# Kernel optimization log

Measured on AMD Instinct MI355X. Metric: run time of the kernel, lower is better.

Reference implementation:

```python
import jax, jax.numpy as jnp
import numpy as np

N, D, H, E, K = 8192, 1024, 4096, 8, 2


def setup_inputs() -> dict:
    key = jax.random.key(0)
    ks = jax.random.split(key, 4)
    scaled = lambda k, shp, fan: (jax.random.normal(k, shp, jnp.float32) / np.sqrt(fan).astype(np.float32))
    return {
        "x": jax.random.normal(ks[0], (N, D), jnp.float32),
        "Wg": scaled(ks[1], (D, E), D),
        "bg": jnp.zeros((E,), jnp.float32),
        "W1": scaled(ks[2], (E, D, H), D),
        "b1": jnp.zeros((E, H), jnp.float32),
        "W2": scaled(ks[3], (E, H, D), H),
        "b2": jnp.zeros((E, D), jnp.float32),
    }


def reference(x, Wg, bg, W1, b1, W2, b2):
    # Gating: softmax over experts, top-k selection, renormalize top-k probs.
    gate_probs = jax.nn.softmax(x @ Wg + bg, axis=-1)            # [N, E]
    topk_p, topk_i = jax.lax.top_k(gate_probs, K)                # [N, K]
    topk_p = topk_p / topk_p.sum(axis=-1, keepdims=True)
    onehot = jax.nn.one_hot(topk_i, E, dtype=x.dtype)            # [N, K, E]
    # Per-token combine weight for each expert (0 if expert not in top-k).
    w = (onehot * topk_p[..., None]).sum(axis=1)                 # [N, E]

    out = jnp.zeros_like(x)
    for e in range(E):  # fixed small loop over structurally distinct experts
        h = jax.nn.relu(x @ W1[e] + b1[e])                       # dropout = identity (eval)
        out = out + w[:, e:e + 1] * (h @ W2[e] + b2[e])

    # Load-balancing auxiliary loss.
    importance = gate_probs.sum(axis=0)
    importance = importance / importance.sum()
    load = onehot.sum(axis=(0, 1)) / (x.shape[0] * K)            # [E]
    lb_loss = E * (importance * load).sum()
    return out, lb_loss
```

## Files before the change

kernel.cpp:

```cpp
#include <hip/hip_runtime.h>
#include <hip/hip_bf16.h>
#include <math.h>

#define NTOK 8192
#define DDIM 1024
#define HDIM 4096
#define NEXP 8
#define KTOP 2
#define MAXROWS 17408
#define MAXTILES 136

typedef __bf16 bf16x8 __attribute__((ext_vector_type(8)));
typedef float f32x4 __attribute__((ext_vector_type(4)));

#define GAS __attribute__((address_space(1)))
#define LAS __attribute__((address_space(3)))

__device__ __forceinline__ void async16(const void* g, void* l) {
  __builtin_amdgcn_global_load_lds((GAS void*)g, (LAS void*)l, 16, 0, 0);
}

#define XB_OFF     ((size_t)0)
#define W1T_OFF    (XB_OFF + (size_t)NTOK*DDIM*2)
#define ROWOUT_OFF W1T_OFF
#define W2T_OFF    (W1T_OFF + (size_t)NEXP*DDIM*HDIM*2)
#define HB_OFF     (W2T_OFF + (size_t)NEXP*HDIM*DDIM*2)
#define ROWTOK_OFF (HB_OFF + (size_t)MAXROWS*HDIM*2)
#define ROWW_OFF   (ROWTOK_OFF + (size_t)MAXROWS*4)
#define TOKE_OFF   (ROWW_OFF + (size_t)MAXROWS*4)
#define TOKW_OFF   (TOKE_OFF + (size_t)NTOK*KTOP*4)
#define TOKROW_OFF (TOKW_OFF + (size_t)NTOK*KTOP*4)
#define TILEE_OFF  (TOKROW_OFF + (size_t)NTOK*KTOP*4)
#define CNT_OFF    (TILEE_OFF + (size_t)256*4)
#define POS_OFF    (CNT_OFF + 64)
#define IMP_OFF    (POS_OFF + 64)
#define META_OFF   (IMP_OFF + 64)

__global__ void init_kernel(int* counts, float* importance) {
  if (threadIdx.x < NEXP) { counts[threadIdx.x] = 0; importance[threadIdx.x] = 0.f; }
}

__global__ void cast_x_kernel(const float* __restrict__ src, __hip_bfloat16* __restrict__ dst) {
  size_t i = ((size_t)blockIdx.x * blockDim.x + threadIdx.x) * 4;
  if (i < (size_t)NTOK * DDIM) {
    float4 v = *(const float4*)(src + i);
    dst[i + 0] = __float2bfloat16(v.x);
    dst[i + 1] = __float2bfloat16(v.y);
    dst[i + 2] = __float2bfloat16(v.z);
    dst[i + 3] = __float2bfloat16(v.w);
  }
}

__global__ __launch_bounds__(256) void transpose_cast_kernel(
    const float* __restrict__ src, __hip_bfloat16* __restrict__ dst, int R, int C) {
  __shared__ float tile[64][65];
  const int e = blockIdx.z;
  const float* s = src + (size_t)e * R * C;
  __hip_bfloat16* d = dst + (size_t)e * R * C;
  const int c0 = blockIdx.x * 64, r0 = blockIdx.y * 64;
  const int tc = (threadIdx.x & 15) * 4;
  const int tr = threadIdx.x >> 4;
#pragma unroll
  for (int p = 0; p < 4; ++p) {
    float4 v = *(const float4*)&s[(size_t)(r0 + tr + p * 16) * C + c0 + tc];
    tile[tr + p * 16][tc + 0] = v.x;
    tile[tr + p * 16][tc + 1] = v.y;
    tile[tr + p * 16][tc + 2] = v.z;
    tile[tr + p * 16][tc + 3] = v.w;
  }
  __syncthreads();
  const int oc = threadIdx.x >> 4;
  const int orr = (threadIdx.x & 15) * 4;
#pragma unroll
  for (int p = 0; p < 4; ++p) {
    const int c = oc + p * 16;
    __hip_bfloat16 tmp[4];
    tmp[0] = __float2bfloat16(tile[orr + 0][c]);
    tmp[1] = __float2bfloat16(tile[orr + 1][c]);
    tmp[2] = __float2bfloat16(tile[orr + 2][c]);
    tmp[3] = __float2bfloat16(tile[orr + 3][c]);
    *(ushort4*)&d[(size_t)(c0 + c) * R + r0 + orr] = *(ushort4*)tmp;
  }
}

__global__ __launch_bounds__(256) void gating_kernel(
    const float* __restrict__ x, const float* __restrict__ Wg, const float* __restrict__ bg,
    int* __restrict__ tok_e, float* __restrict__ tok_w,
    int* __restrict__ counts, float* __restrict__ importance) {
  const int tid = threadIdx.x, wid = tid >> 6, lane = tid & 63;
  const int t = blockIdx.x * 32 + wid * 8 + (lane >> 3);
  const int e = lane & 7;
  const float* xr = x + (size_t)t * DDIM;
  double dot = 0.0;
  for (int d = 0; d < DDIM; d += 4) {
    float4 xv = *(const float4*)(xr + d);
    dot += (double)xv.x * (double)Wg[(d + 0) * NEXP + e];
    dot += (double)xv.y * (double)Wg[(d + 1) * NEXP + e];
    dot += (double)xv.z * (double)Wg[(d + 2) * NEXP + e];
    dot += (double)xv.w * (double)Wg[(d + 3) * NEXP + e];
  }
  double logit = dot + (double)bg[e];
  double m = logit;
  for (int off = 1; off < 8; off <<= 1) {
    double o = __shfl_xor(m, off, 64);
    m = o > m ? o : m;
  }
  double p = exp(logit - m);
  double s = p;
  for (int off = 1; off < 8; off <<= 1) s += __shfl_xor(s, off, 64);
  float prob = (float)(p / s);

  __shared__ float imp[NEXP];
  __shared__ int cnt[NEXP];
  if (tid < NEXP) { imp[tid] = 0.f; cnt[tid] = 0; }
  __syncthreads();
  atomicAdd(&imp[e], prob);

  float bp = prob; int be = e;
  for (int off = 1; off < 8; off <<= 1) {
    float op = __shfl_xor(bp, off, 64); int oe = __shfl_xor(be, off, 64);
    if (op > bp || (op == bp && oe < be)) { bp = op; be = oe; }
  }
  float p2 = (e == be) ? -1.f : prob;
  float sp = p2; int se = e;
  for (int off = 1; off < 8; off <<= 1) {
    float op = __shfl_xor(sp, off, 64); int oe = __shfl_xor(se, off, 64);
    if (op > sp || (op == sp && oe < se)) { sp = op; se = oe; }
  }
  if (e == 0) {
    float tsum = bp + sp;
    tok_e[t * 2 + 0] = be; tok_e[t * 2 + 1] = se;
    tok_w[t * 2 + 0] = bp / tsum; tok_w[t * 2 + 1] = sp / tsum;
    atomicAdd(&cnt[be], 1); atomicAdd(&cnt[se], 1);
  }
  __syncthreads();
  if (tid < NEXP) {
    atomicAdd(&counts[tid], cnt[tid]);
    atomicAdd(&importance[tid], imp[tid]);
  }
}

__global__ void offsets_kernel(const int* __restrict__ counts, int* pos, int* tile_expert,
                               int* meta, int* row_token) {
  if (threadIdx.x == 0) {
    int pb = 0, tb = 0;
    for (int e = 0; e < NEXP; e++) {
      pos[e] = pb;
      int tiles = (counts[e] + 127) >> 7;
      for (int tt = 0; tt < tiles; ++tt) tile_expert[tb + tt] = e;
      pb += tiles * 128; tb += tiles;
    }
    meta[0] = tb;
  }
  __syncthreads();
  for (int i = threadIdx.x; i < MAXROWS; i += blockDim.x) row_token[i] = -1;
}

__global__ void scatter_kernel(const int* __restrict__ tok_e, const float* __restrict__ tok_w,
                               int* __restrict__ pos, int* __restrict__ row_token,
                               float* __restrict__ row_weight, int* __restrict__ tok_row) {
  __shared__ int lcnt[NEXP], lbase[NEXP];
  const int t = blockIdx.x * 256 + threadIdx.x;
  if (threadIdx.x < NEXP) lcnt[threadIdx.x] = 0;
  __syncthreads();
  const int e0 = tok_e[t * 2 + 0], e1 = tok_e[t * 2 + 1];
  const int s0 = atomicAdd(&lcnt[e0], 1);
  const int s1 = atomicAdd(&lcnt[e1], 1);
  __syncthreads();
  if (threadIdx.x < NEXP) lbase[threadIdx.x] = atomicAdd(&pos[threadIdx.x], lcnt[threadIdx.x]);
  __syncthreads();
  int r0 = lbase[e0] + s0; row_token[r0] = t; row_weight[r0] = tok_w[t * 2 + 0]; tok_row[t * 2 + 0] = r0;
  int r1 = lbase[e1] + s1; row_token[r1] = t; row_weight[r1] = tok_w[t * 2 + 1]; tok_row[t * 2 + 1] = r1;
}

__global__ __launch_bounds__(256) void gemm1_kernel(
    const __hip_bfloat16* __restrict__ xb, const __hip_bfloat16* __restrict__ w1t,
    const float* __restrict__ b1, __hip_bfloat16* __restrict__ hb,
    const int* __restrict__ row_token, const int* __restrict__ tile_expert,
    const int* __restrict__ meta) {
  const int tile_y = blockIdx.y;
  if (tile_y >= meta[0]) return;
  const int n0 = blockIdx.x * 128;
  const int e = tile_expert[tile_y];
  const int r0 = tile_y * 128;
  const int tid = threadIdx.x;
  const int wid = tid >> 6, lane = tid & 63;

  __shared__ __align__(16) __hip_bfloat16 As[2][128 * 32];
  __shared__ __align__(16) __hip_bfloat16 Bs[2][128 * 32];

  const int srow = wid * 32 + (lane >> 2);
  const int g = ((lane & 3) ^ (srow & 3)) * 8;
  int t0 = row_token[r0 + srow];      if (t0 < 0) t0 = 0;
  int t1 = row_token[r0 + srow + 16]; if (t1 < 0) t1 = 0;
  const __hip_bfloat16* ga0 = xb + (size_t)t0 * DDIM + g;
  const __hip_bfloat16* ga1 = xb + (size_t)t1 * DDIM + g;
  const __hip_bfloat16* gb0 = w1t + ((size_t)e * HDIM + n0 + srow) * DDIM + g;
  const __hip_bfloat16* gb1 = gb0 + (size_t)16 * DDIM;
  const int ldsA0 = (wid * 32) * 32, ldsA1 = (wid * 32 + 16) * 32;

  f32x4 acc[4][4] = {};
  const int wm = (wid & 1) * 64, wn = (wid >> 1) * 64;
  const int fr = lane & 15;
  const int soff = ((lane >> 4) ^ (lane & 3)) * 8;

#define STAGE1(b) do { \
    async16(ga0, &As[b][ldsA0]); async16(ga1, &As[b][ldsA1]); \
    async16(gb0, &Bs[b][ldsA0]); async16(gb1, &Bs[b][ldsA1]); \
    ga0 += 32; ga1 += 32; gb0 += 32; gb1 += 32; } while (0)

  STAGE1(0);
  for (int kt = 0; kt < DDIM / 32; ++kt) {
    const int cur = kt & 1;
    __syncthreads();
    if (kt + 1 < DDIM / 32) { if (cur) STAGE1(0); else STAGE1(1); }
    bf16x8 av[4], bv[4];
#pragma unroll
    for (int i = 0; i < 4; i++) av[i] = *(const bf16x8*)&As[cur][(wm + i * 16 + fr) * 32 + soff];
#pragma unroll
    for (int j = 0; j < 4; j++) bv[j] = *(const bf16x8*)&Bs[cur][(wn + j * 16 + fr) * 32 + soff];
#pragma unroll
    for (int i = 0; i < 4; i++)
#pragma unroll
      for (int j = 0; j < 4; j++)
        acc[i][j] = __builtin_amdgcn_mfma_f32_16x16x32_bf16(av[i], bv[j], acc[i][j], 0, 0, 0);
  }
#undef STAGE1

  const int crow = (lane >> 4) * 4;
  const int ccol = lane & 15;
#pragma unroll
  for (int j = 0; j < 4; j++) {
    const int gc = n0 + wn + j * 16 + ccol;
    const float bias = b1[e * HDIM + gc];
#pragma unroll
    for (int i = 0; i < 4; i++) {
      const int grb = r0 + wm + i * 16 + crow;
#pragma unroll
      for (int r = 0; r < 4; r++) {
        float v = acc[i][j][r] + bias;
        v = v > 0.f ? v : 0.f;
        hb[(size_t)(grb + r) * HDIM + gc] = __float2bfloat16(v);
      }
    }
  }
}

__global__ __launch_bounds__(256) void gemm2_kernel(
    const __hip_bfloat16* __restrict__ hb, const __hip_bfloat16* __restrict__ w2t,
    const float* __restrict__ b2, __hip_bfloat16* __restrict__ rowout,
    const int* __restrict__ tile_expert, const int* __restrict__ meta) {
  const int tile_y = blockIdx.x % MAXTILES;
  const int cx = blockIdx.x / MAXTILES;
  if (tile_y >= meta[0]) return;
  const int n0 = cx * 128;
  const int e = tile_expert[tile_y];
  const int r0 = tile_y * 128;
  const int tid = threadIdx.x;
  const int wid = tid >> 6, lane = tid & 63;

  __shared__ __align__(16) __hip_bfloat16 As[2][128 * 32];
  __shared__ __align__(16) __hip_bfloat16 Bs[2][128 * 32];

  const int srow = wid * 32 + (lane >> 2);
  const int g = ((lane & 3) ^ (srow & 3)) * 8;
  const __hip_bfloat16* ga0 = hb + ((size_t)r0 + srow) * HDIM + g;
  const __hip_bfloat16* ga1 = ga0 + (size_t)16 * HDIM;
  const __hip_bfloat16* gb0 = w2t + ((size_t)e * DDIM + n0 + srow) * HDIM + g;
  const __hip_bfloat16* gb1 = gb0 + (size_t)16 * HDIM;
  const int ldsA0 = (wid * 32) * 32, ldsA1 = (wid * 32 + 16) * 32;

  f32x4 acc[4][4] = {};
  const int wm = (wid & 1) * 64, wn = (wid >> 1) * 64;
  const int fr = lane & 15;
  const int soff = ((lane >> 4) ^ (lane & 3)) * 8;

#define STAGE2(b) do { \
    async16(ga0, &As[b][ldsA0]); async16(ga1, &As[b][ldsA1]); \
    async16(gb0, &Bs[b][ldsA0]); async16(gb1, &Bs[b][ldsA1]); \
    ga0 += 32; ga1 += 32; gb0 += 32; gb1 += 32; } while (0)

  STAGE2(0);
  for (int kt = 0; kt < HDIM / 32; ++kt) {
    const int cur = kt & 1;
    __syncthreads();
    if (kt + 1 < HDIM / 32) { if (cur) STAGE2(0); else STAGE2(1); }
    bf16x8 av[4], bv[4];
#pragma unroll
    for (int i = 0; i < 4; i++) av[i] = *(const bf16x8*)&As[cur][(wm + i * 16 + fr) * 32 + soff];
#pragma unroll
    for (int j = 0; j < 4; j++) bv[j] = *(const bf16x8*)&Bs[cur][(wn + j * 16 + fr) * 32 + soff];
#pragma unroll
    for (int i = 0; i < 4; i++)
#pragma unroll
      for (int j = 0; j < 4; j++)
        acc[i][j] = __builtin_amdgcn_mfma_f32_16x16x32_bf16(av[i], bv[j], acc[i][j], 0, 0, 0);
  }
#undef STAGE2

  const int crow = (lane >> 4) * 4;
  const int ccol = lane & 15;
#pragma unroll
  for (int j = 0; j < 4; j++) {
    const int gc = n0 + wn + j * 16 + ccol;
    const float bias = b2[e * DDIM + gc];
#pragma unroll
    for (int i = 0; i < 4; i++) {
      const int rr = r0 + wm + i * 16 + crow;
#pragma unroll
      for (int r = 0; r < 4; r++)
        rowout[(size_t)(rr + r) * DDIM + gc] = __float2bfloat16(acc[i][j][r] + bias);
    }
  }
}

__global__ __launch_bounds__(256) void combine_kernel(
    const __hip_bfloat16* __restrict__ rowout, const int* __restrict__ tok_row,
    const float* __restrict__ row_weight, float* __restrict__ out) {
  const int idx = blockIdx.x * 256 + threadIdx.x;
  const int t = idx >> 7;
  const int d = (idx & 127) * 8;
  const int r0 = tok_row[t * 2 + 0], r1 = tok_row[t * 2 + 1];
  const float w0 = row_weight[r0], w1 = row_weight[r1];
  bf16x8 a = *(const bf16x8*)&rowout[(size_t)r0 * DDIM + d];
  bf16x8 b = *(const bf16x8*)&rowout[(size_t)r1 * DDIM + d];
  float o[8];
#pragma unroll
  for (int k = 0; k < 8; k++) o[k] = w0 * (float)a[k] + w1 * (float)b[k];
  float* dst = out + (size_t)t * DDIM + d;
  *(float4*)(dst + 0) = make_float4(o[0], o[1], o[2], o[3]);
  *(float4*)(dst + 4) = make_float4(o[4], o[5], o[6], o[7]);
}

__global__ void finalize_kernel(const float* __restrict__ importance,
                                const int* __restrict__ counts, float* __restrict__ lb_out) {
  if (threadIdx.x == 0 && blockIdx.x == 0) {
    float s = 0.f;
    for (int e = 0; e < NEXP; e++) s += importance[e];
    float lb = 0.f;
    for (int e = 0; e < NEXP; e++)
      lb += (importance[e] / s) * ((float)counts[e] / (float)(NTOK * KTOP));
    lb_out[0] = (float)NEXP * lb;
  }
}

extern "C" void kernel_launch(void* const* d_in, const int* in_sizes, int n_in,
                              void* d_out, int out_size, void* d_ws, size_t ws_size,
                              hipStream_t stream) {
  (void)in_sizes; (void)n_in; (void)out_size; (void)ws_size;
  const float* x  = (const float*)d_in[0];
  const float* Wg = (const float*)d_in[1];
  const float* bg = (const float*)d_in[2];
  const float* W1 = (const float*)d_in[3];
  const float* b1 = (const float*)d_in[4];
  const float* W2 = (const float*)d_in[5];
  const float* b2 = (const float*)d_in[6];
  float* out = (float*)d_out;

  char* ws = (char*)d_ws;
  __hip_bfloat16* xb     = (__hip_bfloat16*)(ws + XB_OFF);
  __hip_bfloat16* w1t    = (__hip_bfloat16*)(ws + W1T_OFF);
  __hip_bfloat16* rowout = (__hip_bfloat16*)(ws + ROWOUT_OFF);
  __hip_bfloat16* w2t    = (__hip_bfloat16*)(ws + W2T_OFF);
  __hip_bfloat16* hb     = (__hip_bfloat16*)(ws + HB_OFF);
  int*   row_token  = (int*)(ws + ROWTOK_OFF);
  float* row_weight = (float*)(ws + ROWW_OFF);
  int*   tok_e   = (int*)(ws + TOKE_OFF);
  float* tok_w   = (float*)(ws + TOKW_OFF);
  int*   tok_row = (int*)(ws + TOKROW_OFF);
  int*   tile_e  = (int*)(ws + TILEE_OFF);
  int*   counts  = (int*)(ws + CNT_OFF);
  int*   pos     = (int*)(ws + POS_OFF);
  float* importance = (float*)(ws + IMP_OFF);
  int*   meta    = (int*)(ws + META_OFF);

  init_kernel<<<1, 64, 0, stream>>>(counts, importance);
  cast_x_kernel<<<NTOK * DDIM / 4 / 256, 256, 0, stream>>>(x, xb);
  transpose_cast_kernel<<<dim3(HDIM / 64, DDIM / 64, NEXP), 256, 0, stream>>>(W1, w1t, DDIM, HDIM);
  transpose_cast_kernel<<<dim3(DDIM / 64, HDIM / 64, NEXP), 256, 0, stream>>>(W2, w2t, HDIM, DDIM);
  gating_kernel<<<NTOK / 32, 256, 0, stream>>>(x, Wg, bg, tok_e, tok_w, counts, importance);
  offsets_kernel<<<1, 256, 0, stream>>>(counts, pos, tile_e, meta, row_token);
  scatter_kernel<<<NTOK / 256, 256, 0, stream>>>(tok_e, tok_w, pos, row_token, row_weight, tok_row);
  gemm1_kernel<<<dim3(HDIM / 128, MAXTILES), 256, 0, stream>>>(xb, w1t, b1, hb, row_token, tile_e, meta);
  gemm2_kernel<<<dim3((DDIM / 128) * MAXTILES), 256, 0, stream>>>(hb, w2t, b2, rowout, tile_e, meta);
  combine_kernel<<<NTOK * 128 / 256, 256, 0, stream>>>(rowout, tok_row, row_weight, out);
  finalize_kernel<<<1, 64, 0, stream>>>(importance, counts, out + (size_t)NTOK * DDIM);
}
```

Baseline: 820.5 us.

## Deepen both expert GEMMs to a four-stage async LDS pipeline with explicit waitcnt

Both grouped GEMM kernels move from double buffering to a four-slot LDS ring, prefetching two K-tiles ahead. They wait with an explicit s_waitcnt vmcnt(8) and a single s_barrier per iteration instead of __syncthreads, which drains all loads. MFMA blocks run at raised wave priority and are fenced with sched_barrier. The aim is to keep more global loads in flight and hide memory latency behind matrix math. The cost is doubled LDS per block (64 KB), which may lower occupancy. The last iterations also issue redundant loads so the vmcnt counting stays uniform.

```diff
diff --git a/kernel.cpp b/kernel.cpp
--- a/kernel.cpp
+++ b/kernel.cpp
@@ -186,8 +186,8 @@
   const int tid = threadIdx.x;
   const int wid = tid >> 6, lane = tid & 63;
 
-  __shared__ __align__(16) __hip_bfloat16 As[2][128 * 32];
-  __shared__ __align__(16) __hip_bfloat16 Bs[2][128 * 32];
+  __shared__ __align__(16) __hip_bfloat16 As[4][128 * 32];
+  __shared__ __align__(16) __hip_bfloat16 Bs[4][128 * 32];
 
   const int srow = wid * 32 + (lane >> 2);
   const int g = ((lane & 3) ^ (srow & 3)) * 8;
@@ -203,29 +203,40 @@
   const int wm = (wid & 1) * 64, wn = (wid >> 1) * 64;
   const int fr = lane & 15;
   const int soff = ((lane >> 4) ^ (lane & 3)) * 8;
+  const int NT = DDIM / 32;
 
 #define STAGE1(b) do { \
     async16(ga0, &As[b][ldsA0]); async16(ga1, &As[b][ldsA1]); \
-    async16(gb0, &Bs[b][ldsA0]); async16(gb1, &Bs[b][ldsA1]); \
-    ga0 += 32; ga1 += 32; gb0 += 32; gb1 += 32; } while (0)
-
-  STAGE1(0);
-  for (int kt = 0; kt < DDIM / 32; ++kt) {
-    const int cur = kt & 1;
-    __syncthreads();
-    if (kt + 1 < DDIM / 32) { if (cur) STAGE1(0); else STAGE1(1); }
+    async16(gb0, &Bs[b][ldsA0]); async16(gb1, &Bs[b][ldsA1]); } while (0)
+#define ADV1 do { ga0 += 32; ga1 += 32; gb0 += 32; gb1 += 32; } while (0)
+
+  STAGE1(0); ADV1;
+  STAGE1(1); ADV1;
+  for (int kt = 0; kt < NT; ++kt) {
+    STAGE1((kt + 2) & 3);
+    if (kt + 3 < NT) ADV1;
+    asm volatile("s_waitcnt vmcnt(8)" ::: "memory");
+    __builtin_amdgcn_s_barrier();
+    asm volatile("" ::: "memory");
+    __builtin_amdgcn_sched_barrier(0);
+    const int cur = kt & 3;
     bf16x8 av[4], bv[4];
 #pragma unroll
     for (int i = 0; i < 4; i++) av[i] = *(const bf16x8*)&As[cur][(wm + i * 16 + fr) * 32 + soff];
 #pragma unroll
     for (int j = 0; j < 4; j++) bv[j] = *(const bf16x8*)&Bs[cur][(wn + j * 16 + fr) * 32 + soff];
+    __builtin_amdgcn_s_setprio(1);
 #pragma unroll
     for (int i = 0; i < 4; i++)
 #pragma unroll
       for (int j = 0; j < 4; j++)
         acc[i][j] = __builtin_amdgcn_mfma_f32_16x16x32_bf16(av[i], bv[j], acc[i][j], 0, 0, 0);
+    __builtin_amdgcn_s_setprio(0);
+    __builtin_amdgcn_sched_barrier(0);
   }
 #undef STAGE1
+#undef ADV1
+  asm volatile("s_waitcnt vmcnt(0)" ::: "memory");
 
   const int crow = (lane >> 4) * 4;
   const int ccol = lane & 15;
@@ -259,8 +270,8 @@
   const int tid = threadIdx.x;
   const int wid = tid >> 6, lane = tid & 63;
 
-  __shared__ __align__(16) __hip_bfloat16 As[2][128 * 32];
-  __shared__ __align__(16) __hip_bfloat16 Bs[2][128 * 32];
+  __shared__ __align__(16) __hip_bfloat16 As[4][128 * 32];
+  __shared__ __align__(16) __hip_bfloat16 Bs[4][128 * 32];
 
   const int srow = wid * 32 + (lane >> 2);
   const int g = ((lane & 3) ^ (srow & 3)) * 8;
@@ -274,29 +285,40 @@
   const int wm = (wid & 1) * 64, wn = (wid >> 1) * 64;
   const int fr = lane & 15;
   const int soff = ((lane >> 4) ^ (lane & 3)) * 8;
+  const int NT = HDIM / 32;
 
 #define STAGE2(b) do { \
     async16(ga0, &As[b][ldsA0]); async16(ga1, &As[b][ldsA1]); \
-    async16(gb0, &Bs[b][ldsA0]); async16(gb1, &Bs[b][ldsA1]); \
-    ga0 += 32; ga1 += 32; gb0 += 32; gb1 += 32; } while (0)
-
-  STAGE2(0);
-  for (int kt = 0; kt < HDIM / 32; ++kt) {
-    const int cur = kt & 1;
-    __syncthreads();
-    if (kt + 1 < HDIM / 32) { if (cur) STAGE2(0); else STAGE2(1); }
+    async16(gb0, &Bs[b][ldsA0]); async16(gb1, &Bs[b][ldsA1]); } while (0)
+#define ADV2 do { ga0 += 32; ga1 += 32; gb0 += 32; gb1 += 32; } while (0)
+
+  STAGE2(0); ADV2;
+  STAGE2(1); ADV2;
+  for (int kt = 0; kt < NT; ++kt) {
+    STAGE2((kt + 2) & 3);
+    if (kt + 3 < NT) ADV2;
+    asm volatile("s_waitcnt vmcnt(8)" ::: "memory");
+    __builtin_amdgcn_s_barrier();
+    asm volatile("" ::: "memory");
+    __builtin_amdgcn_sched_barrier(0);
+    const int cur = kt & 3;
     bf16x8 av[4], bv[4];
 #pragma unroll
     for (int i = 0; i < 4; i++) av[i] = *(const bf16x8*)&As[cur][(wm + i * 16 + fr) * 32 + soff];
 #pragma unroll
     for (int j = 0; j < 4; j++) bv[j] = *(const bf16x8*)&Bs[cur][(wn + j * 16 + fr) * 32 + soff];
+    __builtin_amdgcn_s_setprio(1);
 #pragma unroll
     for (int i = 0; i < 4; i++)
 #pragma unroll
       for (int j = 0; j < 4; j++)
         acc[i][j] = __builtin_amdgcn_mfma_f32_16x16x32_bf16(av[i], bv[j], acc[i][j], 0, 0, 0);
+    __builtin_amdgcn_s_setprio(0);
+    __builtin_amdgcn_sched_barrier(0);
   }
 #undef STAGE2
+#undef ADV2
+  asm volatile("s_waitcnt vmcnt(0)" ::: "memory");
 
   const int crow = (lane >> 4) * 4;
   const int ccol = lane & 15;
```

Result: slower. 874.1 us (+6.5%).
